# Kernel tuning notes

Hardware: AMD Instinct MI355X
Metric: run time of the kernel (lower is better)

Reference implementation:

```python
import jax, jax.numpy as jnp
import numpy as np

NEG_SLOPE = 0.2


def gat_layer(h, src, dst, W, al, ar, b, num_nodes):
    # h: [N, Din], W: [Din, H*F], al/ar: [H, F], b: [H*F]
    H, F = al.shape
    feat = (h @ W).reshape(-1, H, F)                      # [N, H, F]
    el = jnp.sum(feat * al[None], axis=-1)                # [N, H]
    er = jnp.sum(feat * ar[None], axis=-1)                # [N, H]
    e = el[src] + er[dst]                                 # [E, H]
    e = jnp.where(e > 0, e, NEG_SLOPE * e)                # leaky_relu(0.2)
    # edge softmax over incoming edges of each dst node (per head)
    m = jax.ops.segment_max(e, dst, num_segments=num_nodes)   # [N, H]
    m = jnp.where(jnp.isfinite(m), m, 0.0)
    a = jnp.exp(e - m[dst])                               # [E, H]
    s = jax.ops.segment_sum(a, dst, num_segments=num_nodes)   # [N, H]
    alpha = a / jnp.maximum(s[dst], 1e-9)                 # [E, H]
    msg = feat[src] * alpha[:, :, None]                   # [E, H, F]
    out = jax.ops.segment_sum(msg, dst, num_segments=num_nodes)  # [N, H, F]
    out = out + b.reshape(H, F)[None]
    return out.reshape(-1, H * F)                         # view(-1, H*F)


def setup_inputs() -> dict:
    key = jax.random.key(0)
    ks = jax.random.split(key, 16)
    N, E, Din, Hh, F = 50000, 800000, 256, 4, 64
    s = 0.05
    return {
        "h": jax.random.normal(ks[0], (N, Din), jnp.float32),
        "src": jax.random.randint(ks[1], (E,), 0, N),
        "dst": jax.random.randint(ks[2], (E,), 0, N),
        "dst_node_ids": jax.random.randint(ks[3], (1024,), 0, N),
        "W0": jax.random.normal(ks[4], (Din, Hh * F), jnp.float32) * s,
        "al0": jax.random.normal(ks[5], (Hh, F), jnp.float32) * s,
        "ar0": jax.random.normal(ks[6], (Hh, F), jnp.float32) * s,
        "b0": jnp.zeros((Hh * F,), jnp.float32),
        "W1": jax.random.normal(ks[7], (Hh * F, Hh * F), jnp.float32) * s,
        "al1": jax.random.normal(ks[8], (Hh, F), jnp.float32) * s,
        "ar1": jax.random.normal(ks[9], (Hh, F), jnp.float32) * s,
        "b1": jnp.zeros((Hh * F,), jnp.float32),
        "W2": jax.random.normal(ks[10], (Hh * F, F), jnp.float32) * s,
        "al2": jax.random.normal(ks[11], (1, F), jnp.float32) * s,
        "ar2": jax.random.normal(ks[12], (1, F), jnp.float32) * s,
        "b2": jnp.zeros((F,), jnp.float32),
    }


def reference(h, src, dst, dst_node_ids,
              W0, al0, ar0, b0, W1, al1, ar1, b1, W2, al2, ar2, b2):
    N = h.shape[0]
    h = h.astype(jnp.float32)
    h = gat_layer(h, src, dst, W0, al0, ar0, b0, N)
    h = gat_layer(h, src, dst, W1, al1, ar1, b1, N)
    h = gat_layer(h, src, dst, W2, al2, ar2, b2, N)
    return h, dst_node_ids
```

## Files before the change

kernel.cpp:

```cpp
#include <hip/hip_runtime.h>
#include <hip/hip_bf16.h>

#define NEG_SLOPE 0.2f

typedef __attribute__((ext_vector_type(8))) short bf16x8;
typedef __attribute__((ext_vector_type(4))) float f32x4;

static inline int cdiv(int a, int b) { return (a + b - 1) / b; }

__device__ inline unsigned short f2bf(float x) {
  __hip_bfloat16 b = __float2bfloat16(x);
  return *reinterpret_cast<unsigned short*>(&b);
}
__device__ inline float bf2f(unsigned short u) {
  unsigned int v = (unsigned int)u << 16;
  return *reinterpret_cast<float*>(&v);
}

__global__ void splitT_all(const float* __restrict__ W0, unsigned short* __restrict__ W0hi,
                           const float* __restrict__ W1, unsigned short* __restrict__ W1hi,
                           const float* __restrict__ W2, unsigned short* __restrict__ W2hi) {
  const int S0 = 256 * 256, S1 = 256 * 256, S2 = 256 * 64;
  int i = blockIdx.x * blockDim.x + threadIdx.x;
  const float* W; unsigned short* hi; int K, Mo, perm;
  if (i < S0) { W = W0; hi = W0hi; K = 256; Mo = 256; perm = 0; }
  else if (i < S0 + S1) { i -= S0; W = W1; hi = W1hi; K = 256; Mo = 256; perm = 1; }
  else if (i < S0 + S1 + S2) { i -= S0 + S1; W = W2; hi = W2hi; K = 256; Mo = 64; perm = 1; }
  else return;
  int k = i / Mo, m = i - k * Mo;
  int kk = perm ? ((k & 63) * 4 + (k >> 6)) : k;
  hi[(size_t)m * K + kk] = f2bf(W[i]);
}

template <int NF, bool CVT>
__global__ __launch_bounds__(256) void gemm_split(
    const unsigned short* __restrict__ Ahi, const float* __restrict__ Af32,
    const unsigned short* __restrict__ BThi,
    unsigned short* __restrict__ Chi,
    const float* __restrict__ alv, const float* __restrict__ arv,
    float* __restrict__ el, float* __restrict__ er, int Hn, int M, int K, int Ncols) {
  constexpr int BN = NF * 32;
  __shared__ unsigned short As[128][40];
  __shared__ unsigned short Bs[BN][40];
  const int tid = threadIdx.x;
  const int row0 = blockIdx.x * 128;
  const int col0 = blockIdx.y * BN;
  const int wid = tid >> 6, lane = tid & 63;
  const int wm = wid >> 1, wn = wid & 1;
  const int l15 = lane & 15, lg = lane >> 4;
  f32x4 acc[4][NF];
#pragma unroll
  for (int m = 0; m < 4; ++m)
#pragma unroll
    for (int n = 0; n < NF; ++n) acc[m][n] = (f32x4){0.f, 0.f, 0.f, 0.f};

  const uint4 zero4 = {0u, 0u, 0u, 0u};
  for (int k0 = 0; k0 < K; k0 += 32) {
    {
      int r = tid >> 2;
      const int kg = tid & 3;
#pragma unroll
      for (int it = 0; it < 2; ++it, r += 64) {
        const int grow = row0 + r;
        if constexpr (CVT) {
          float4 f0 = make_float4(0.f, 0.f, 0.f, 0.f), f1 = f0;
          if (grow < M) {
            f0 = *reinterpret_cast<const float4*>(&Af32[(size_t)grow * K + k0 + kg * 8]);
            f1 = *reinterpret_cast<const float4*>(&Af32[(size_t)grow * K + k0 + kg * 8 + 4]);
          }
          unsigned short t[8];
          t[0] = f2bf(f0.x); t[1] = f2bf(f0.y); t[2] = f2bf(f0.z); t[3] = f2bf(f0.w);
          t[4] = f2bf(f1.x); t[5] = f2bf(f1.y); t[6] = f2bf(f1.z); t[7] = f2bf(f1.w);
          *reinterpret_cast<uint4*>(&As[r][kg * 8]) = *reinterpret_cast<const uint4*>(t);
        } else {
          uint4 vh = zero4;
          if (grow < M) vh = *reinterpret_cast<const uint4*>(&Ahi[(size_t)grow * K + k0 + kg * 8]);
          *reinterpret_cast<uint4*>(&As[r][kg * 8]) = vh;
        }
      }
    }
    {
      int r = tid >> 2;
      const int kg = tid & 3;
#pragma unroll
      for (int it = 0; it < BN / 64; ++it, r += 64) {
        const int gcol = col0 + r;
        uint4 vh = *reinterpret_cast<const uint4*>(&BThi[(size_t)gcol * K + k0 + kg * 8]);
        *reinterpret_cast<uint4*>(&Bs[r][kg * 8]) = vh;
      }
    }
    __syncthreads();
    bf16x8 ah[4];
#pragma unroll
    for (int m = 0; m < 4; ++m) {
      const int row = wm * 64 + m * 16 + l15;
      ah[m] = *reinterpret_cast<const bf16x8*>(&As[row][lg * 8]);
    }
#pragma unroll
    for (int n = 0; n < NF; ++n) {
      const int col = wn * (NF * 16) + n * 16 + l15;
      bf16x8 bh = *reinterpret_cast<const bf16x8*>(&Bs[col][lg * 8]);
#pragma unroll
      for (int m = 0; m < 4; ++m)
        acc[m][n] = __builtin_amdgcn_mfma_f32_16x16x32_bf16(ah[m], bh, acc[m][n], 0, 0, 0);
    }
    __syncthreads();
  }
  const int hw = (col0 + wn * (NF * 16)) >> 6;
  float alw[NF], arw[NF];
#pragma unroll
  for (int n = 0; n < NF; ++n) {
    const int colg = col0 + wn * (NF * 16) + n * 16 + l15;
    alw[n] = alv[colg];
    arw[n] = arv[colg];
  }
  float pel[4][4] = {{0.f}}, per_[4][4] = {{0.f}};
#pragma unroll
  for (int m = 0; m < 4; ++m) {
#pragma unroll
    for (int n = 0; n < NF; ++n) {
      const int col = col0 + wn * (NF * 16) + n * 16 + l15;
#pragma unroll
      for (int j = 0; j < 4; ++j) {
        const int row = row0 + wm * 64 + m * 16 + lg * 4 + j;
        const float v = acc[m][n][j];
        if (row < M) {
          if constexpr (NF == 4) {
            Chi[(size_t)row * 256 + (col & 63) * 4 + (col >> 6)] = f2bf(v);
          } else {
            Chi[(size_t)row * Ncols + col] = f2bf(v);
          }
        }
        pel[m][j] = fmaf(v, alw[n], pel[m][j]);
        per_[m][j] = fmaf(v, arw[n], per_[m][j]);
      }
    }
  }
  float rl[4][4], rr[4][4];
#pragma unroll
  for (int m = 0; m < 4; ++m) {
#pragma unroll
    for (int j = 0; j < 4; ++j) {
      float vl = pel[m][j], vr = per_[m][j];
#pragma unroll
      for (int off = 1; off < 16; off <<= 1) {
        vl += __shfl_xor(vl, off);
        vr += __shfl_xor(vr, off);
      }
      rl[m][j] = vl; rr[m][j] = vr;
    }
  }
  if constexpr (NF == 4) {
    if (l15 == 0) {
#pragma unroll
      for (int m = 0; m < 4; ++m)
#pragma unroll
        for (int j = 0; j < 4; ++j) {
          const int row = row0 + wm * 64 + m * 16 + lg * 4 + j;
          if (row < M) {
            el[(size_t)row * 4 + hw] = rl[m][j];
            er[(size_t)row * 4 + hw] = rr[m][j];
          }
        }
    }
  } else {
    __shared__ float sl[128], sr[128];
    if (wn == 1 && l15 == 0) {
#pragma unroll
      for (int m = 0; m < 4; ++m)
#pragma unroll
        for (int j = 0; j < 4; ++j) {
          const int lr = wm * 64 + m * 16 + lg * 4 + j;
          sl[lr] = rl[m][j]; sr[lr] = rr[m][j];
        }
    }
    __syncthreads();
    if (wn == 0 && l15 == 0) {
#pragma unroll
      for (int m = 0; m < 4; ++m)
#pragma unroll
        for (int j = 0; j < 4; ++j) {
          const int lr = wm * 64 + m * 16 + lg * 4 + j;
          const int row = row0 + lr;
          if (row < M) {
            el[row] = rl[m][j] + sl[lr];
            er[row] = rr[m][j] + sr[lr];
          }
        }
    }
  }
}

__global__ void hist_kernel(const int* __restrict__ dst, int* __restrict__ deg, int E) {
  int i = blockIdx.x * blockDim.x + threadIdx.x;
  if (i < E) atomicAdd(&deg[dst[i]], 1);
}

__global__ void scan1(const int* __restrict__ deg, int* __restrict__ offs,
                      int* __restrict__ bsums, int N) {
  __shared__ int tmp[256];
  const int tid = threadIdx.x;
  const int i = blockIdx.x * 256 + tid;
  int v = (i < N) ? deg[i] : 0;
  tmp[tid] = v;
  __syncthreads();
  for (int d = 1; d < 256; d <<= 1) {
    int t = (tid >= d) ? tmp[tid - d] : 0;
    __syncthreads();
    tmp[tid] += t;
    __syncthreads();
  }
  if (i < N) offs[i] = tmp[tid] - v;
  if (tid == 255) bsums[blockIdx.x] = tmp[255];
}

__global__ void scan2(int* __restrict__ bsums, int nb) {
  __shared__ int tmp[256];
  const int tid = threadIdx.x;
  int v = (tid < nb) ? bsums[tid] : 0;
  tmp[tid] = v;
  __syncthreads();
  for (int d = 1; d < 256; d <<= 1) {
    int t = (tid >= d) ? tmp[tid - d] : 0;
    __syncthreads();
    tmp[tid] += t;
    __syncthreads();
  }
  if (tid < nb) bsums[tid] = tmp[tid] - v;
}

__global__ void scan3(int* __restrict__ offs, const int* __restrict__ bsums,
                      int* __restrict__ cursor, int N, int E) {
  const int i = blockIdx.x * 256 + threadIdx.x;
  if (i < N) {
    const int v = offs[i] + bsums[blockIdx.x];
    offs[i] = v;
    cursor[i] = v;
  }
  if (i == 0) offs[N] = E;
}

__global__ void scatter_kernel(const int* __restrict__ src, const int* __restrict__ dst,
                               int* __restrict__ cursor, int* __restrict__ csr_src, int E) {
  int i = blockIdx.x * blockDim.x + threadIdx.x;
  if (i >= E) return;
  int pos = atomicAdd(&cursor[dst[i]], 1);
  csr_src[pos] = src[i];
}

template <int H>
__global__ void alpha16(const int* __restrict__ offs, const int* __restrict__ csr_src,
                        const float* __restrict__ el, const float* __restrict__ er,
                        unsigned short* __restrict__ abuf, int N) {
  const int w = (int)((blockIdx.x * (size_t)blockDim.x + threadIdx.x) >> 6);
  const int lane = threadIdx.x & 63;
  const int g = lane >> 4, q = lane & 15;
  const int node = w * 4 + g;
  int beg = 0, end = 0;
  float erh[H];
#pragma unroll
  for (int h = 0; h < H; ++h) erh[h] = 0.f;
  if (node < N) {
    beg = offs[node]; end = offs[node + 1];
    if constexpr (H == 4) {
      float4 t = *reinterpret_cast<const float4*>(&er[(size_t)node * 4]);
      erh[0] = t.x; erh[1] = t.y; erh[2] = t.z; erh[3] = t.w;
    } else {
      erh[0] = er[node];
    }
  }
  float m[H], s[H];
#pragma unroll
  for (int h = 0; h < H; ++h) { m[h] = -INFINITY; s[h] = 0.f; }
  for (int i0 = beg; i0 < end; i0 += 16) {
    const int i = i0 + q;
    const bool valid = i < end;
    const int sn = valid ? csr_src[i] : 0;
    float e[H];
    if constexpr (H == 4) {
      float4 v = *reinterpret_cast<const float4*>(&el[(size_t)sn * 4]);
      e[0] = v.x + erh[0]; e[1] = v.y + erh[1]; e[2] = v.z + erh[2]; e[3] = v.w + erh[3];
    } else {
      e[0] = el[sn] + erh[0];
    }
#pragma unroll
    for (int h = 0; h < H; ++h) {
      e[h] = e[h] > 0.f ? e[h] : NEG_SLOPE * e[h];
      if (!valid) e[h] = -INFINITY;
      float cm = e[h];
#pragma unroll
      for (int off = 1; off < 16; off <<= 1) cm = fmaxf(cm, __shfl_xor(cm, off));
      const float nm = fmaxf(m[h], cm);
      float cs = __expf(e[h] - nm);
#pragma unroll
      for (int off = 1; off < 16; off <<= 1) cs += __shfl_xor(cs, off);
      s[h] = s[h] * __expf(m[h] - nm) + cs;
      m[h] = nm;
    }
  }
  float inv[H];
#pragma unroll
  for (int h = 0; h < H; ++h) inv[h] = 1.f / fmaxf(s[h], 1e-9f);
  for (int i0 = beg; i0 < end; i0 += 16) {
    const int i = i0 + q;
    if (i < end) {
      const int sn = csr_src[i];
      float e[H];
      if constexpr (H == 4) {
        float4 v = *reinterpret_cast<const float4*>(&el[(size_t)sn * 4]);
        e[0] = v.x + erh[0]; e[1] = v.y + erh[1]; e[2] = v.z + erh[2]; e[3] = v.w + erh[3];
      } else {
        e[0] = el[sn] + erh[0];
      }
#pragma unroll
      for (int h = 0; h < H; ++h) {
        e[h] = e[h] > 0.f ? e[h] : NEG_SLOPE * e[h];
        e[h] = __expf(e[h] - m[h]) * inv[h];
      }
      if constexpr (H == 4) {
        ushort4 o;
        o.x = f2bf(e[0]); o.y = f2bf(e[1]); o.z = f2bf(e[2]); o.w = f2bf(e[3]);
        *reinterpret_cast<ushort4*>(&abuf[(size_t)i * 4]) = o;
      } else {
        abuf[i] = f2bf(e[0]);
      }
    }
  }
}

__global__ void aggregate_h4(const int* __restrict__ offs, const int* __restrict__ csr_src,
                             const ushort4* __restrict__ feat4, const ushort4* __restrict__ abuf4,
                             const float* __restrict__ bias, ushort4* __restrict__ out4, int N) {
  const int node = (int)((blockIdx.x * (size_t)blockDim.x + threadIdx.x) >> 6);
  const int lane = threadIdx.x & 63;
  if (node >= N) return;
  const int beg = offs[node], end = offs[node + 1];
  float a0 = 0.f, a1 = 0.f, a2 = 0.f, a3 = 0.f;
  int i = beg;
  for (; i + 7 < end; i += 8) {
    int sn[8]; ushort4 w[8]; ushort4 uv[8];
#pragma unroll
    for (int u = 0; u < 8; ++u) sn[u] = csr_src[i + u];
#pragma unroll
    for (int u = 0; u < 8; ++u) w[u] = abuf4[i + u];
#pragma unroll
    for (int u = 0; u < 8; ++u) uv[u] = feat4[(size_t)sn[u] * 64 + lane];
#pragma unroll
    for (int u = 0; u < 8; ++u) {
      a0 = fmaf(bf2f(w[u].x), bf2f(uv[u].x), a0);
      a1 = fmaf(bf2f(w[u].y), bf2f(uv[u].y), a1);
      a2 = fmaf(bf2f(w[u].z), bf2f(uv[u].z), a2);
      a3 = fmaf(bf2f(w[u].w), bf2f(uv[u].w), a3);
    }
  }
  for (; i < end; ++i) {
    const int sn = csr_src[i];
    const ushort4 w = abuf4[i];
    const ushort4 uv = feat4[(size_t)sn * 64 + lane];
    a0 = fmaf(bf2f(w.x), bf2f(uv.x), a0);
    a1 = fmaf(bf2f(w.y), bf2f(uv.y), a1);
    a2 = fmaf(bf2f(w.z), bf2f(uv.z), a2);
    a3 = fmaf(bf2f(w.w), bf2f(uv.w), a3);
  }
  const float o0 = a0 + bias[lane];
  const float o1 = a1 + bias[64 + lane];
  const float o2 = a2 + bias[128 + lane];
  const float o3 = a3 + bias[192 + lane];
  ushort4 ov;
  ov.x = f2bf(o0); ov.y = f2bf(o1); ov.z = f2bf(o2); ov.w = f2bf(o3);
  out4[(size_t)node * 64 + lane] = ov;
}

__global__ void aggregate1(const int* __restrict__ offs, const int* __restrict__ csr_src,
                           const unsigned short* __restrict__ featH, const unsigned short* __restrict__ abuf,
                           const float* __restrict__ bias, float* __restrict__ outf, int N) {
  const int wid = (int)((blockIdx.x * (size_t)blockDim.x + threadIdx.x) >> 6);
  const int lane = threadIdx.x & 63;
  if (wid >= N) return;
  const int beg = offs[wid], end = offs[wid + 1];
  const int g = lane >> 4, q = lane & 15;
  float4 acc = make_float4(0.f, 0.f, 0.f, 0.f);
  for (int i0 = beg; i0 < end; i0 += 4) {
    const int e = i0 + g;
    if (e < end) {
      const int sn = csr_src[e];
      const float a = bf2f(abuf[e]);
      const ushort4 u = *reinterpret_cast<const ushort4*>(&featH[(size_t)sn * 64 + q * 4]);
      acc.x = fmaf(a, bf2f(u.x), acc.x);
      acc.y = fmaf(a, bf2f(u.y), acc.y);
      acc.z = fmaf(a, bf2f(u.z), acc.z);
      acc.w = fmaf(a, bf2f(u.w), acc.w);
    }
  }
#pragma unroll
  for (int off = 16; off <= 32; off <<= 1) {
    acc.x += __shfl_xor(acc.x, off);
    acc.y += __shfl_xor(acc.y, off);
    acc.z += __shfl_xor(acc.z, off);
    acc.w += __shfl_xor(acc.w, off);
  }
  if (lane < 16) {
    const float4 b4 = *reinterpret_cast<const float4*>(&bias[q * 4]);
    float4 o = make_float4(acc.x + b4.x, acc.y + b4.y, acc.z + b4.z, acc.w + b4.w);
    *reinterpret_cast<float4*>(&outf[(size_t)wid * 64 + q * 4]) = o;
  }
}

__global__ void copy_ids(const int* __restrict__ ids, float* __restrict__ out, int n) {
  int i = blockIdx.x * blockDim.x + threadIdx.x;
  if (i < n) out[i] = (float)ids[i];
}

extern "C" void kernel_launch(void* const* d_in, const int* in_sizes, int n_in,
                              void* d_out, int out_size, void* d_ws, size_t ws_size,
                              hipStream_t stream) {
  const float* h   = (const float*)d_in[0];
  const int* src   = (const int*)d_in[1];
  const int* dst   = (const int*)d_in[2];
  const int* ids   = (const int*)d_in[3];
  const float* W0  = (const float*)d_in[4];
  const float* al0 = (const float*)d_in[5];
  const float* ar0 = (const float*)d_in[6];
  const float* b0  = (const float*)d_in[7];
  const float* W1  = (const float*)d_in[8];
  const float* al1 = (const float*)d_in[9];
  const float* ar1 = (const float*)d_in[10];
  const float* b1  = (const float*)d_in[11];
  const float* W2  = (const float*)d_in[12];
  const float* al2 = (const float*)d_in[13];
  const float* ar2 = (const float*)d_in[14];
  const float* b2  = (const float*)d_in[15];

  const int Din = 256, HF = 256, F2 = 64;
  const int N = in_sizes[0] / Din;
  const int E = in_sizes[1];
  const int NIDS = in_sizes[3];

  char* p = (char*)d_ws;
  unsigned short* Chi = (unsigned short*)p; p += (size_t)N * 256 * 2;
  unsigned short* Ahi = (unsigned short*)p; p += (size_t)N * 256 * 2;
  unsigned short* W0hi = (unsigned short*)p; p += (size_t)HF * Din * 2;
  unsigned short* W1hi = (unsigned short*)p; p += (size_t)HF * HF * 2;
  unsigned short* W2hi = (unsigned short*)p; p += (size_t)F2 * HF * 2;
  float* el   = (float*)p;             p += (size_t)N * 4 * 4;
  float* er   = (float*)p;             p += (size_t)N * 4 * 4;
  unsigned short* abuf = (unsigned short*)p; p += (size_t)E * 4 * 2;
  int* deg    = (int*)p;               p += (size_t)N * 4;
  int* offs   = (int*)p;               p += (size_t)(N + 16) * 4;
  int* bsums  = (int*)p;               p += 256 * 4;
  int* csr_src = (int*)p;              p += (size_t)E * 4;

  float* outp = (float*)d_out;
  dim3 blk(256);
  const int nb = cdiv(N, 256);
  const int nwAlpha = cdiv(cdiv(N, 4) * 64, 256);

  splitT_all<<<cdiv(256 * 256 * 2 + 256 * 64, 256), blk, 0, stream>>>(
      W0, W0hi, W1, W1hi, W2, W2hi);

  hipMemsetAsync(deg, 0, (size_t)N * 4, stream);
  hist_kernel<<<cdiv(E, 256), blk, 0, stream>>>(dst, deg, E);
  scan1<<<nb, blk, 0, stream>>>(deg, offs, bsums, N);
  scan2<<<1, blk, 0, stream>>>(bsums, nb);
  scan3<<<nb, blk, 0, stream>>>(offs, bsums, deg, N, E);
  scatter_kernel<<<cdiv(E, 256), blk, 0, stream>>>(src, dst, deg, csr_src, E);

  {
    dim3 g(cdiv(N, 128), HF / 128);
    gemm_split<4, true><<<g, blk, 0, stream>>>(nullptr, h, W0hi, Chi, al0, ar0, el, er, 4, N, Din, HF);
    alpha16<4><<<nwAlpha, blk, 0, stream>>>(offs, csr_src, el, er, abuf, N);
    aggregate_h4<<<cdiv(N * 64, 256), blk, 0, stream>>>(offs, csr_src, (const ushort4*)Chi,
                                                        (const ushort4*)abuf, b0, (ushort4*)Ahi, N);
  }
  {
    dim3 g(cdiv(N, 128), HF / 128);
    gemm_split<4, false><<<g, blk, 0, stream>>>(Ahi, nullptr, W1hi, Chi, al1, ar1, el, er, 4, N, HF, HF);
    alpha16<4><<<nwAlpha, blk, 0, stream>>>(offs, csr_src, el, er, abuf, N);
    aggregate_h4<<<cdiv(N * 64, 256), blk, 0, stream>>>(offs, csr_src, (const ushort4*)Chi,
                                                        (const ushort4*)abuf, b1, (ushort4*)Ahi, N);
  }
  {
    dim3 g(cdiv(N, 128), 1);
    gemm_split<2, false><<<g, blk, 0, stream>>>(Ahi, nullptr, W2hi, Chi, al2, ar2, el, er, 1, N, HF, F2);
    alpha16<1><<<nwAlpha, blk, 0, stream>>>(offs, csr_src, el, er, abuf, N);
    aggregate1<<<cdiv(N * 64, 256), blk, 0, stream>>>(offs, csr_src, Chi, abuf, b2, outp, N);
  }
  copy_ids<<<cdiv(NIDS, 256), blk, 0, stream>>>(ids, outp + (size_t)N * F2, NIDS);
}
```

Baseline: 389.3 us.

## Quantize per-head GAT features to int8 with per-row scale folded into alpha

For the two 4-head layers, the GEMM epilogue now writes projected features as int8 with a per-row, per-head absmax scale instead of bf16. The scale is stored next to el, and the softmax kernel multiplies it into each edge weight, so aggregation dequantizes for free. This halves the bytes of the random per-edge feature gathers, which dominate aggregation traffic. The cost is int8 precision loss in hidden-layer features, which may push the output past the accuracy tolerance.

```diff
diff --git a/kernel.cpp b/kernel.cpp
--- a/kernel.cpp
+++ b/kernel.cpp
@@ -36,9 +36,11 @@
 __global__ __launch_bounds__(256) void gemm_split(
     const unsigned short* __restrict__ Ahi, const float* __restrict__ Af32,
     const unsigned short* __restrict__ BThi,
-    unsigned short* __restrict__ Chi,
+    unsigned short* __restrict__ Chi, signed char* __restrict__ Cq,
     const float* __restrict__ alv, const float* __restrict__ arv,
-    float* __restrict__ el, float* __restrict__ er, int Hn, int M, int K, int Ncols) {
+    float* __restrict__ elsc, float* __restrict__ er4,
+    float* __restrict__ el1, float* __restrict__ er1,
+    int M, int K, int Ncols) {
   constexpr int BN = NF * 32;
   __shared__ unsigned short As[128][40];
   __shared__ unsigned short Bs[BN][40];
@@ -114,56 +116,74 @@
     alw[n] = alv[colg];
     arw[n] = arv[colg];
   }
-  float pel[4][4] = {{0.f}}, per_[4][4] = {{0.f}};
-#pragma unroll
-  for (int m = 0; m < 4; ++m) {
-#pragma unroll
-    for (int n = 0; n < NF; ++n) {
-      const int col = col0 + wn * (NF * 16) + n * 16 + l15;
+
+  if constexpr (NF == 4) {
+#pragma unroll
+    for (int m = 0; m < 4; ++m) {
 #pragma unroll
       for (int j = 0; j < 4; ++j) {
+        float mx = 0.f, vl = 0.f, vr = 0.f;
+#pragma unroll
+        for (int n = 0; n < 4; ++n) {
+          const float v = acc[m][n][j];
+          mx = fmaxf(mx, fabsf(v));
+          vl = fmaf(v, alw[n], vl);
+          vr = fmaf(v, arw[n], vr);
+        }
+#pragma unroll
+        for (int off = 1; off < 16; off <<= 1) {
+          mx = fmaxf(mx, __shfl_xor(mx, off));
+          vl += __shfl_xor(vl, off);
+          vr += __shfl_xor(vr, off);
+        }
         const int row = row0 + wm * 64 + m * 16 + lg * 4 + j;
-        const float v = acc[m][n][j];
         if (row < M) {
-          if constexpr (NF == 4) {
-            Chi[(size_t)row * 256 + (col & 63) * 4 + (col >> 6)] = f2bf(v);
-          } else {
-            Chi[(size_t)row * Ncols + col] = f2bf(v);
+          const float rinv = mx > 0.f ? 127.f / mx : 0.f;
+#pragma unroll
+          for (int n = 0; n < 4; ++n) {
+            const int f = n * 16 + l15;
+            const int q = __float2int_rn(acc[m][n][j] * rinv);
+            Cq[(size_t)row * 256 + (f << 2) + hw] = (signed char)q;
           }
-        }
-        pel[m][j] = fmaf(v, alw[n], pel[m][j]);
-        per_[m][j] = fmaf(v, arw[n], per_[m][j]);
+          if (l15 == 0) {
+            elsc[(size_t)row * 8 + hw] = vl;
+            elsc[(size_t)row * 8 + 4 + hw] = mx * (1.f / 127.f);
+            er4[(size_t)row * 4 + hw] = vr;
+          }
+        }
       }
     }
-  }
-  float rl[4][4], rr[4][4];
-#pragma unroll
-  for (int m = 0; m < 4; ++m) {
-#pragma unroll
-    for (int j = 0; j < 4; ++j) {
-      float vl = pel[m][j], vr = per_[m][j];
-#pragma unroll
-      for (int off = 1; off < 16; off <<= 1) {
-        vl += __shfl_xor(vl, off);
-        vr += __shfl_xor(vr, off);
-      }
-      rl[m][j] = vl; rr[m][j] = vr;
-    }
-  }
-  if constexpr (NF == 4) {
-    if (l15 == 0) {
-#pragma unroll
-      for (int m = 0; m < 4; ++m)
+  } else {
+    float pel[4][4] = {{0.f}}, per_[4][4] = {{0.f}};
+#pragma unroll
+    for (int m = 0; m < 4; ++m) {
+#pragma unroll
+      for (int n = 0; n < NF; ++n) {
+        const int col = col0 + wn * (NF * 16) + n * 16 + l15;
 #pragma unroll
         for (int j = 0; j < 4; ++j) {
           const int row = row0 + wm * 64 + m * 16 + lg * 4 + j;
-          if (row < M) {
-            el[(size_t)row * 4 + hw] = rl[m][j];
-            er[(size_t)row * 4 + hw] = rr[m][j];
-          }
-        }
-    }
-  } else {
+          const float v = acc[m][n][j];
+          if (row < M) Chi[(size_t)row * Ncols + col] = f2bf(v);
+          pel[m][j] = fmaf(v, alw[n], pel[m][j]);
+          per_[m][j] = fmaf(v, arw[n], per_[m][j]);
+        }
+      }
+    }
+    float rl[4][4], rr[4][4];
+#pragma unroll
+    for (int m = 0; m < 4; ++m) {
+#pragma unroll
+      for (int j = 0; j < 4; ++j) {
+        float vl = pel[m][j], vr = per_[m][j];
+#pragma unroll
+        for (int off = 1; off < 16; off <<= 1) {
+          vl += __shfl_xor(vl, off);
+          vr += __shfl_xor(vr, off);
+        }
+        rl[m][j] = vl; rr[m][j] = vr;
+      }
+    }
     __shared__ float sl[128], sr[128];
     if (wn == 1 && l15 == 0) {
 #pragma unroll
@@ -183,8 +203,8 @@
           const int lr = wm * 64 + m * 16 + lg * 4 + j;
           const int row = row0 + lr;
           if (row < M) {
-            el[row] = rl[m][j] + sl[lr];
-            er[row] = rr[m][j] + sr[lr];
+            el1[row] = rl[m][j] + sl[lr];
+            er1[row] = rr[m][j] + sr[lr];
           }
         }
     }
@@ -248,43 +268,31 @@
   csr_src[pos] = src[i];
 }
 
-template <int H>
-__global__ void alpha16(const int* __restrict__ offs, const int* __restrict__ csr_src,
-                        const float* __restrict__ el, const float* __restrict__ er,
-                        unsigned short* __restrict__ abuf, int N) {
+__global__ void alpha16_h4(const int* __restrict__ offs, const int* __restrict__ csr_src,
+                           const float* __restrict__ elsc, const float* __restrict__ er4,
+                           unsigned short* __restrict__ abuf, int N) {
   const int w = (int)((blockIdx.x * (size_t)blockDim.x + threadIdx.x) >> 6);
   const int lane = threadIdx.x & 63;
   const int g = lane >> 4, q = lane & 15;
   const int node = w * 4 + g;
   int beg = 0, end = 0;
-  float erh[H];
-#pragma unroll
-  for (int h = 0; h < H; ++h) erh[h] = 0.f;
+  float erh[4] = {0.f, 0.f, 0.f, 0.f};
   if (node < N) {
     beg = offs[node]; end = offs[node + 1];
-    if constexpr (H == 4) {
-      float4 t = *reinterpret_cast<const float4*>(&er[(size_t)node * 4]);
-      erh[0] = t.x; erh[1] = t.y; erh[2] = t.z; erh[3] = t.w;
-    } else {
-      erh[0] = er[node];
-    }
-  }
-  float m[H], s[H];
-#pragma unroll
-  for (int h = 0; h < H; ++h) { m[h] = -INFINITY; s[h] = 0.f; }
+    float4 t = *reinterpret_cast<const float4*>(&er4[(size_t)node * 4]);
+    erh[0] = t.x; erh[1] = t.y; erh[2] = t.z; erh[3] = t.w;
+  }
+  float m[4], s[4];
+#pragma unroll
+  for (int h = 0; h < 4; ++h) { m[h] = -INFINITY; s[h] = 0.f; }
   for (int i0 = beg; i0 < end; i0 += 16) {
     const int i = i0 + q;
     const bool valid = i < end;
     const int sn = valid ? csr_src[i] : 0;
-    float e[H];
-    if constexpr (H == 4) {
-      float4 v = *reinterpret_cast<const float4*>(&el[(size_t)sn * 4]);
-      e[0] = v.x + erh[0]; e[1] = v.y + erh[1]; e[2] = v.z + erh[2]; e[3] = v.w + erh[3];
-    } else {
-      e[0] = el[sn] + erh[0];
-    }
-#pragma unroll
-    for (int h = 0; h < H; ++h) {
+    float4 v = *reinterpret_cast<const float4*>(&elsc[(size_t)sn * 8]);
+    float e[4] = {v.x + erh[0], v.y + erh[1], v.z + erh[2], v.w + erh[3]};
+#pragma unroll
+    for (int h = 0; h < 4; ++h) {
       e[h] = e[h] > 0.f ? e[h] : NEG_SLOPE * e[h];
       if (!valid) e[h] = -INFINITY;
       float cm = e[h];
@@ -298,38 +306,71 @@
       m[h] = nm;
     }
   }
-  float inv[H];
-#pragma unroll
-  for (int h = 0; h < H; ++h) inv[h] = 1.f / fmaxf(s[h], 1e-9f);
+  float inv[4];
+#pragma unroll
+  for (int h = 0; h < 4; ++h) inv[h] = 1.f / fmaxf(s[h], 1e-9f);
   for (int i0 = beg; i0 < end; i0 += 16) {
     const int i = i0 + q;
     if (i < end) {
       const int sn = csr_src[i];
-      float e[H];
-      if constexpr (H == 4) {
-        float4 v = *reinterpret_cast<const float4*>(&el[(size_t)sn * 4]);
-        e[0] = v.x + erh[0]; e[1] = v.y + erh[1]; e[2] = v.z + erh[2]; e[3] = v.w + erh[3];
-      } else {
-        e[0] = el[sn] + erh[0];
+      float4 v = *reinterpret_cast<const float4*>(&elsc[(size_t)sn * 8]);
+      float4 sc = *reinterpret_cast<const float4*>(&elsc[(size_t)sn * 8 + 4]);
+      float e[4] = {v.x + erh[0], v.y + erh[1], v.z + erh[2], v.w + erh[3]};
+      const float scv[4] = {sc.x, sc.y, sc.z, sc.w};
+#pragma unroll
+      for (int h = 0; h < 4; ++h) {
+        e[h] = e[h] > 0.f ? e[h] : NEG_SLOPE * e[h];
+        e[h] = __expf(e[h] - m[h]) * inv[h] * scv[h];
       }
-#pragma unroll
-      for (int h = 0; h < H; ++h) {
-        e[h] = e[h] > 0.f ? e[h] : NEG_SLOPE * e[h];
-        e[h] = __expf(e[h] - m[h]) * inv[h];
-      }
-      if constexpr (H == 4) {
-        ushort4 o;
-        o.x = f2bf(e[0]); o.y = f2bf(e[1]); o.z = f2bf(e[2]); o.w = f2bf(e[3]);
-        *reinterpret_cast<ushort4*>(&abuf[(size_t)i * 4]) = o;
-      } else {
-        abuf[i] = f2bf(e[0]);
-      }
+      ushort4 o;
+      o.x = f2bf(e[0]); o.y = f2bf(e[1]); o.z = f2bf(e[2]); o.w = f2bf(e[3]);
+      *reinterpret_cast<ushort4*>(&abuf[(size_t)i * 4]) = o;
+    }
+  }
+}
+
+__global__ void alpha16_h1(const int* __restrict__ offs, const int* __restrict__ csr_src,
+                           const float* __restrict__ el, const float* __restrict__ er,
+                           unsigned short* __restrict__ abuf, int N) {
+  const int w = (int)((blockIdx.x * (size_t)blockDim.x + threadIdx.x) >> 6);
+  const int lane = threadIdx.x & 63;
+  const int g = lane >> 4, q = lane & 15;
+  const int node = w * 4 + g;
+  int beg = 0, end = 0;
+  float erh = 0.f;
+  if (node < N) { beg = offs[node]; end = offs[node + 1]; erh = er[node]; }
+  float m = -INFINITY, s = 0.f;
+  for (int i0 = beg; i0 < end; i0 += 16) {
+    const int i = i0 + q;
+    const bool valid = i < end;
+    const int sn = valid ? csr_src[i] : 0;
+    float e = el[sn] + erh;
+    e = e > 0.f ? e : NEG_SLOPE * e;
+    if (!valid) e = -INFINITY;
+    float cm = e;
+#pragma unroll
+    for (int off = 1; off < 16; off <<= 1) cm = fmaxf(cm, __shfl_xor(cm, off));
+    const float nm = fmaxf(m, cm);
+    float cs = __expf(e - nm);
+#pragma unroll
+    for (int off = 1; off < 16; off <<= 1) cs += __shfl_xor(cs, off);
+    s = s * __expf(m - nm) + cs;
+    m = nm;
+  }
+  const float inv = 1.f / fmaxf(s, 1e-9f);
+  for (int i0 = beg; i0 < end; i0 += 16) {
+    const int i = i0 + q;
+    if (i < end) {
+      const int sn = csr_src[i];
+      float e = el[sn] + erh;
+      e = e > 0.f ? e : NEG_SLOPE * e;
+      abuf[i] = f2bf(__expf(e - m) * inv);
     }
   }
 }
 
 __global__ void aggregate_h4(const int* __restrict__ offs, const int* __restrict__ csr_src,
-                             const ushort4* __restrict__ feat4, const ushort4* __restrict__ abuf4,
+                             const unsigned* __restrict__ qtab, const ushort4* __restrict__ abuf4,
                              const float* __restrict__ bias, ushort4* __restrict__ out4, int N) {
   const int node = (int)((blockIdx.x * (size_t)blockDim.x + threadIdx.x) >> 6);
   const int lane = threadIdx.x & 63;
@@ -338,29 +379,29 @@
   float a0 = 0.f, a1 = 0.f, a2 = 0.f, a3 = 0.f;
   int i = beg;
   for (; i + 7 < end; i += 8) {
-    int sn[8]; ushort4 w[8]; ushort4 uv[8];
+    int sn[8]; ushort4 w[8]; unsigned qw[8];
 #pragma unroll
     for (int u = 0; u < 8; ++u) sn[u] = csr_src[i + u];
 #pragma unroll
     for (int u = 0; u < 8; ++u) w[u] = abuf4[i + u];
 #pragma unroll
-    for (int u = 0; u < 8; ++u) uv[u] = feat4[(size_t)sn[u] * 64 + lane];
+    for (int u = 0; u < 8; ++u) qw[u] = qtab[(size_t)sn[u] * 64 + lane];
 #pragma unroll
     for (int u = 0; u < 8; ++u) {
-      a0 = fmaf(bf2f(w[u].x), bf2f(uv[u].x), a0);
-      a1 = fmaf(bf2f(w[u].y), bf2f(uv[u].y), a1);
-      a2 = fmaf(bf2f(w[u].z), bf2f(uv[u].z), a2);
-      a3 = fmaf(bf2f(w[u].w), bf2f(uv[u].w), a3);
+      a0 = fmaf(bf2f(w[u].x), (float)(int)(signed char)(qw[u] & 0xff), a0);
+      a1 = fmaf(bf2f(w[u].y), (float)(int)(signed char)((qw[u] >> 8) & 0xff), a1);
+      a2 = fmaf(bf2f(w[u].z), (float)(int)(signed char)((qw[u] >> 16) & 0xff), a2);
+      a3 = fmaf(bf2f(w[u].w), (float)(int)(signed char)(qw[u] >> 24), a3);
     }
   }
   for (; i < end; ++i) {
     const int sn = csr_src[i];
     const ushort4 w = abuf4[i];
-    const ushort4 uv = feat4[(size_t)sn * 64 + lane];
-    a0 = fmaf(bf2f(w.x), bf2f(uv.x), a0);
-    a1 = fmaf(bf2f(w.y), bf2f(uv.y), a1);
-    a2 = fmaf(bf2f(w.z), bf2f(uv.z), a2);
-    a3 = fmaf(bf2f(w.w), bf2f(uv.w), a3);
+    const unsigned qw = qtab[(size_t)sn * 64 + lane];
+    a0 = fmaf(bf2f(w.x), (float)(int)(signed char)(qw & 0xff), a0);
+    a1 = fmaf(bf2f(w.y), (float)(int)(signed char)((qw >> 8) & 0xff), a1);
+    a2 = fmaf(bf2f(w.z), (float)(int)(signed char)((qw >> 16) & 0xff), a2);
+    a3 = fmaf(bf2f(w.w), (float)(int)(signed char)(qw >> 24), a3);
   }
   const float o0 = a0 + bias[lane];
   const float o1 = a1 + bias[64 + lane];
@@ -437,13 +478,16 @@
   const int NIDS = in_sizes[3];
 
   char* p = (char*)d_ws;
-  unsigned short* Chi = (unsigned short*)p; p += (size_t)N * 256 * 2;
+  signed char* Cq = (signed char*)p;   p += (size_t)N * 256;
+  unsigned short* Chi = (unsigned short*)p; p += (size_t)N * 64 * 2;
   unsigned short* Ahi = (unsigned short*)p; p += (size_t)N * 256 * 2;
   unsigned short* W0hi = (unsigned short*)p; p += (size_t)HF * Din * 2;
   unsigned short* W1hi = (unsigned short*)p; p += (size_t)HF * HF * 2;
   unsigned short* W2hi = (unsigned short*)p; p += (size_t)F2 * HF * 2;
-  float* el   = (float*)p;             p += (size_t)N * 4 * 4;
-  float* er   = (float*)p;             p += (size_t)N * 4 * 4;
+  float* elsc = (float*)p;             p += (size_t)N * 8 * 4;
+  float* er4  = (float*)p;             p += (size_t)N * 4 * 4;
+  float* el1  = (float*)p;             p += (size_t)N * 4;
+  float* er1  = (float*)p;             p += (size_t)N * 4;
   unsigned short* abuf = (unsigned short*)p; p += (size_t)E * 4 * 2;
   int* deg    = (int*)p;               p += (size_t)N * 4;
   int* offs   = (int*)p;               p += (size_t)(N + 16) * 4;
@@ -467,22 +511,25 @@
 
   {
     dim3 g(cdiv(N, 128), HF / 128);
-    gemm_split<4, true><<<g, blk, 0, stream>>>(nullptr, h, W0hi, Chi, al0, ar0, el, er, 4, N, Din, HF);
-    alpha16<4><<<nwAlpha, blk, 0, stream>>>(offs, csr_src, el, er, abuf, N);
-    aggregate_h4<<<cdiv(N * 64, 256), blk, 0, stream>>>(offs, csr_src, (const ushort4*)Chi,
+    gemm_split<4, true><<<g, blk, 0, stream>>>(nullptr, h, W0hi, nullptr, Cq, al0, ar0,
+                                               elsc, er4, nullptr, nullptr, N, Din, HF);
+    alpha16_h4<<<nwAlpha, blk, 0, stream>>>(offs, csr_src, elsc, er4, abuf, N);
+    aggregate_h4<<<cdiv(N * 64, 256), blk, 0, stream>>>(offs, csr_src, (const unsigned*)Cq,
                                                         (const ushort4*)abuf, b0, (ushort4*)Ahi, N);
   }
   {
     dim3 g(cdiv(N, 128), HF / 128);
-    gemm_split<4, false><<<g, blk, 0, stream>>>(Ahi, nullptr, W1hi, Chi, al1, ar1, el, er, 4, N, HF, HF);
-    alpha16<4><<<nwAlpha, blk, 0, stream>>>(offs, csr_src, el, er, abuf, N);
-    aggregate_h4<<<cdiv(N * 64, 256), blk, 0, stream>>>(offs, csr_src, (const ushort4*)Chi,
+    gemm_split<4, false><<<g, blk, 0, stream>>>(Ahi, nullptr, W1hi, nullptr, Cq, al1, ar1,
+                                                elsc, er4, nullptr, nullptr, N, HF, HF);
+    alpha16_h4<<<nwAlpha, blk, 0, stream>>>(offs, csr_src, elsc, er4, abuf, N);
+    aggregate_h4<<<cdiv(N * 64, 256), blk, 0, stream>>>(offs, csr_src, (const unsigned*)Cq,
                                                         (const ushort4*)abuf, b1, (ushort4*)Ahi, N);
   }
   {
     dim3 g(cdiv(N, 128), 1);
-    gemm_split<2, false><<<g, blk, 0, stream>>>(Ahi, nullptr, W2hi, Chi, al2, ar2, el, er, 1, N, HF, F2);
-    alpha16<1><<<nwAlpha, blk, 0, stream>>>(offs, csr_src, el, er, abuf, N);
+    gemm_split<2, false><<<g, blk, 0, stream>>>(Ahi, nullptr, W2hi, Chi, nullptr, al2, ar2,
+                                                nullptr, nullptr, el1, er1, N, HF, F2);
+    alpha16_h1<<<nwAlpha, blk, 0, stream>>>(offs, csr_src, el1, er1, abuf, N);
     aggregate1<<<cdiv(N * 64, 256), blk, 0, stream>>>(offs, csr_src, Chi, abuf, b2, outp, N);
   }
   copy_ids<<<cdiv(NIDS, 256), blk, 0, stream>>>(ids, outp + (size_t)N * F2, NIDS);
```

New measurement: 361.8 us. -7.1%, faster.
